# Performance work log

Hardware: AMD Instinct MI355X
Metric: run time of the kernel (lower is better)

Reference implementation:

```python
import jax, jax.numpy as jnp
import numpy as np

K = 3          # opt.k: number of nearest SOM nodes each point is assigned to
SOM_M = 256    # opt.node_num (16x16 SOM grid)


def _point_resnet(x, ws, bs):
    # SO-Net PointResNet: stack of 1x1 conv (relu) layers; the LAST layer takes
    # concat(prev_out, input) as a residual skip connection.
    out = x
    n = len(ws)
    for i in range(n):
        inp = jnp.concatenate([out, x], axis=1) if i == n - 1 else out
        out = jax.nn.relu(jnp.einsum('oc,bcn->bon', ws[i], inp) + bs[i][None, :, None])
    return out


def _encoder(x, sn, node, fp_ws, fp_bs, fn_ws, fn_bs):
    B, _, N = x.shape
    M = node.shape[2]
    xd = jax.lax.stop_gradient(x)      # torch used x.data throughout SOM logic
    nd = jax.lax.stop_gradient(node)
    # squared distances point->node: B,N,M
    x2 = jnp.sum(xd * xd, axis=1)
    n2 = jnp.sum(nd * nd, axis=1)
    cross = jnp.einsum('bcn,bcm->bnm', xd, nd)
    d2 = x2[:, :, None] + n2[:, None, :] - 2.0 * cross
    _, knn_idx = jax.lax.top_k(-d2, K)                 # B,N,K nearest SOM nodes
    min_idx = jnp.transpose(knn_idx, (0, 2, 1)).reshape(B, K * N)  # B,kN (k-major, matches x_stack)
    x_stack = jnp.tile(x, (1, 1, K))                   # B,3,kN
    xs_d = jax.lax.stop_gradient(x_stack)
    # mask_row_sum (counts per node) and masked sum == one-hot mask multiply in the original
    counts = jax.vmap(lambda s: jax.ops.segment_sum(jnp.ones(s.shape, jnp.float32), s, num_segments=SOM_M))(min_idx)  # B,M
    sums = jax.vmap(lambda d, s: jax.ops.segment_sum(d, s, num_segments=SOM_M))(jnp.transpose(xs_d, (0, 2, 1)), min_idx)  # B,M,3
    cluster_mean = jnp.transpose(sums, (0, 2, 1)) / (counts[:, None, :] + 1e-5)  # B,3,M (new som_node)
    # centers: per-point gather of its assigned node (sum(mask*node) over M)
    centers = jnp.take_along_axis(cluster_mean, min_idx[:, None, :], axis=2)     # B,3,kN
    x_dec = jax.lax.stop_gradient(x_stack - centers)   # .detach() in original
    first = _point_resnet(x_dec, fp_ws, fp_bs)         # B,384,kN
    # index_max + gather: per (b,c,node) max over assigned points; empty nodes -> point index 0
    node_max = jax.vmap(lambda d, s: jax.ops.segment_max(d, s, num_segments=SOM_M))(jnp.transpose(first, (0, 2, 1)), min_idx)  # B,M,C
    node_max = jnp.transpose(node_max, (0, 2, 1))      # B,C,M
    has_pts = counts > 0                               # mask_row_max
    fallback = first[:, :, 0:1]                        # gather index 0 for empty nodes
    masked_max = jnp.where(has_pts[:, None, :], node_max, fallback)  # B,384,M
    final_in = jnp.concatenate([cluster_mean, masked_max], axis=1)   # B,387,M
    final = _point_resnet(final_in, fn_ws, fn_bs)      # B,1024,M
    return jnp.max(final, axis=2)                      # B,1024 global feature


def setup_inputs() -> dict:
    key = jax.random.key(0)
    ks = jax.random.split(key, 24)
    B, N, M = 8, 4096, SOM_M
    inp = {
        'x': jax.random.normal(ks[0], (B, 3, N), jnp.float32),
        'sn': jax.random.normal(ks[1], (B, 3, N), jnp.float32),
        'node': jax.random.normal(ks[2], (B, 3, M), jnp.float32),
        'node_knn_I': jax.random.randint(ks[3], (B, M, 1), 0, M),
    }
    fp_dims = [(3, 64), (64, 128), (128, 256), (256 + 3, 384)]
    fn_dims = [(387, 512), (512, 512), (512, 768), (768 + 387, 1024)]
    i = 4
    for j, (cin, cout) in enumerate(fp_dims):
        inp[f'fp_w{j}'] = jax.random.normal(ks[i], (cout, cin), jnp.float32) * np.float32(np.sqrt(2.0 / cin)); i += 1
        inp[f'fp_b{j}'] = jnp.zeros((cout,), jnp.float32)
    for j, (cin, cout) in enumerate(fn_dims):
        inp[f'fn_w{j}'] = jax.random.normal(ks[i], (cout, cin), jnp.float32) * np.float32(np.sqrt(2.0 / cin)); i += 1
        inp[f'fn_b{j}'] = jnp.zeros((cout,), jnp.float32)
    return inp


def reference(x, sn, node, node_knn_I,
              fp_w0, fp_b0, fp_w1, fp_b1, fp_w2, fp_b2, fp_w3, fp_b3,
              fn_w0, fn_b0, fn_w1, fn_b1, fn_w2, fn_b2, fn_w3, fn_b3):
    fp_ws = [fp_w0, fp_w1, fp_w2, fp_w3]
    fp_bs = [fp_b0, fp_b1, fp_b2, fp_b3]
    fn_ws = [fn_w0, fn_w1, fn_w2, fn_w3]
    fn_bs = [fn_b0, fn_b1, fn_b2, fn_b3]
    # node_knn_I only used when som_k >= 2 (KNNModule); som_k=1 here.
    return _encoder(x, sn, node, fp_ws, fp_bs, fn_ws, fn_bs)
```

## Files before the change

### kernel.cpp

```cpp
#include <hip/hip_runtime.h>
#include <math.h>

#define B_   8
#define N_   4096
#define M_   256
#define KNN_ 3

#define OFF_COUNTS   0
#define OFF_CM       8192
#define OFF_NODEMAX  14336
#define OFF_H0       14336
#define OFF_FIRST0   800768
#define OFF_KNN      807944
#define OFF_CAT      807944
#define OFF_SORTED   906248
#define OFF_MSORT    1004552
#define OFF_FIN2     2020360
#define OFF_H1       2020360
#define OFF_WBF      2544648
#define OFF_W3X      3661832
#define O_W0 0
#define O_W1 2048
#define O_W2 10240
#define O_W3 43008
#define O_V0 153600
#define O_V1 366592
#define O_V2 628736
#define O_V3 1021952
#define W_TOTAL 2234368

typedef short  bf16x8 __attribute__((ext_vector_type(8)));
typedef float  f32x4  __attribute__((ext_vector_type(4)));
typedef float  f32x16 __attribute__((ext_vector_type(16)));

__device__ __forceinline__ unsigned short f2b(float f) {
    unsigned u = __float_as_uint(f);
    return (unsigned short)((u + 0x7FFFu + ((u >> 16) & 1u)) >> 16);
}
__device__ __forceinline__ unsigned cvt2(float lo, float hi) {
    unsigned r;
    asm("v_cvt_pk_bf16_f32 %0, %1, %2" : "=v"(r) : "v"(lo), "v"(hi));
    return r;
}
__device__ __forceinline__ f32x16 zero16() {
    f32x16 z;
    #pragma unroll
    for (int i = 0; i < 16; i++) z[i] = 0.f;
    return z;
}

__global__ __launch_bounds__(256) void knn_setup(
        const float* __restrict__ x, const float* __restrict__ node,
        int* __restrict__ knn,
        const float* s0, const float* s1, const float* s2, const float* s3,
        const float* s4, const float* s5, const float* s6, const float* s7,
        unsigned short* __restrict__ dst, float* __restrict__ w3x) {
    __shared__ float nd0[M_], nd1[M_], nd2[M_], nn2[M_];
    int t = threadIdx.x;
    if (blockIdx.x < 128) {
        int b = blockIdx.x >> 4, xblk = blockIdx.x & 15;
        {
            float c0 = node[(b * 3 + 0) * M_ + t];
            float c1 = node[(b * 3 + 1) * M_ + t];
            float c2 = node[(b * 3 + 2) * M_ + t];
            nd0[t] = c0; nd1[t] = c1; nd2[t] = c2;
            nn2[t] = c0 * c0 + c1 * c1 + c2 * c2;
        }
        __syncthreads();
        int n = xblk * 256 + t;
        float x0 = x[(b * 3 + 0) * N_ + n];
        float x1 = x[(b * 3 + 1) * N_ + n];
        float x2 = x[(b * 3 + 2) * N_ + n];
        float xx = x0 * x0 + x1 * x1 + x2 * x2;
        float d0 = 1e30f, d1 = 1e30f, d2b = 1e30f;
        int i0 = 0, i1 = 0, i2 = 0;
        for (int m = 0; m < M_; m++) {
            float cross = x0 * nd0[m] + x1 * nd1[m] + x2 * nd2[m];
            float d = xx + nn2[m] - 2.f * cross;
            bool c0 = d < d0, c1 = d < d1, c2 = d < d2b;
            d2b = c1 ? d1 : (c2 ? d : d2b);
            i2  = c1 ? i1 : (c2 ? m : i2);
            d1  = c0 ? d0 : (c1 ? d : d1);
            i1  = c0 ? i0 : (c1 ? m : i1);
            d0  = c0 ? d  : d0;
            i0  = c0 ? m  : i0;
        }
        int base = (b * N_ + n) * 3;
        knn[base + 0] = i0; knn[base + 1] = i1; knn[base + 2] = i2;
    } else {
        int i = (blockIdx.x - 128) * 256 + t;
        int st = (gridDim.x - 128) * 256;
        for (int j = i; j < 1536; j += st) {
            int ch = j >> 2, c = j & 3;
            w3x[j] = (c < 3) ? s3[ch * 259 + 256 + c] : 0.f;
        }
        for (; i < W_TOTAL; i += st) {
            unsigned short v;
            if (i < O_W1) {
                int loc = i, co = loc >> 5, k = loc & 31;
                v = (k < 3) ? f2b(s0[co * 3 + k]) : (unsigned short)0;
            } else if (i < O_W2) {
                int loc = i - O_W1, co = loc >> 6, k = loc & 63;
                v = f2b(s1[co * 64 + k]);
            } else if (i < O_W3) {
                int loc = i - O_W2, co = loc >> 7, k = loc & 127;
                v = f2b(s2[co * 128 + k]);
            } else if (i < O_V0) {
                int loc = i - O_W3, co = loc / 288u, k = loc - co * 288;
                v = (k < 259) ? f2b(s3[co * 259 + k]) : (unsigned short)0;
            } else if (i < O_V1) {
                int loc = i - O_V0, co = loc / 416u, k = loc - co * 416;
                v = (k < 387) ? f2b(s4[co * 387 + k]) : (unsigned short)0;
            } else if (i < O_V2) {
                int loc = i - O_V1, co = loc >> 9, k = loc & 511;
                v = f2b(s5[co * 512 + k]);
            } else if (i < O_V3) {
                int loc = i - O_V2, co = loc >> 9, k = loc & 511;
                v = f2b(s6[co * 512 + k]);
            } else {
                int loc = i - O_V3, co = loc / 1184u, k = loc - co * 1184;
                v = (k < 1155) ? f2b(s7[co * 1155 + k]) : (unsigned short)0;
            }
            dst[i] = v;
        }
    }
}

__global__ __launch_bounds__(256) void prep(const float* __restrict__ x,
        const int* __restrict__ knn, float* __restrict__ counts_g,
        float* __restrict__ cm, int* __restrict__ sorted, int* __restrict__ msort) {
    __shared__ float hs0[256], hs1[256], hs2[256];
    __shared__ int hc[256], tmp[256], offsL[257], cur[256];
    int t = threadIdx.x, b = blockIdx.x;
    hs0[t] = 0.f; hs1[t] = 0.f; hs2[t] = 0.f; hc[t] = 0; cur[t] = 0;
    __syncthreads();
    for (int e = t; e < KNN_ * N_; e += 256) {
        int n = e & (N_ - 1), k = e >> 12;
        int m = knn[(b * N_ + n) * 3 + k];
        (void)k;
        atomicAdd(&hc[m], 1);
        atomicAdd(&hs0[m], x[(b * 3 + 0) * N_ + n]);
        atomicAdd(&hs1[m], x[(b * 3 + 1) * N_ + n]);
        atomicAdd(&hs2[m], x[(b * 3 + 2) * N_ + n]);
    }
    __syncthreads();
    int v = hc[t];
    float cnt = (float)v;
    counts_g[b * M_ + t] = cnt;
    float inv = 1.f / (cnt + 1e-5f);
    cm[(b * 3 + 0) * M_ + t] = hs0[t] * inv;
    cm[(b * 3 + 1) * M_ + t] = hs1[t] * inv;
    cm[(b * 3 + 2) * M_ + t] = hs2[t] * inv;
    tmp[t] = v;
    __syncthreads();
    for (int off = 1; off < 256; off <<= 1) {
        int u = (t >= off) ? tmp[t - off] : 0;
        __syncthreads();
        tmp[t] += u;
        __syncthreads();
    }
    offsL[t] = tmp[t] - v;
    if (t == 255) offsL[256] = tmp[255];
    __syncthreads();
    for (int e = t; e < KNN_ * N_; e += 256) {
        int n = e & (N_ - 1), k = e >> 12;
        int m = knn[(b * N_ + n) * 3 + k];
        int pos = atomicAdd(&cur[m], 1);
        int dst = offsL[m] + pos;
        sorted[b * (KNN_ * N_) + dst] = e;
        msort[b * (KNN_ * N_) + dst] = m;
    }
}

template<int KS, int INS, int OUTS, int CTW>
__device__ __forceinline__ void layerB(const unsigned short* __restrict__ Wg,
        const float* __restrict__ bias, const unsigned short* actin,
        unsigned short* actout, int wave, int lane) {
    int r = lane & 15, g = lane >> 4;
    bf16x8 bfr[4][KS];
    #pragma unroll
    for (int pt = 0; pt < 4; pt++) {
        const unsigned short* arow = actin + (pt * 16 + r) * INS + g * 8;
        #pragma unroll
        for (int ks = 0; ks < KS; ks++)
            bfr[pt][ks] = *(const bf16x8*)(arow + ks * 32);
    }
    #pragma unroll
    for (int c = 0; c < CTW; c++) {
        int ct = wave * CTW + c;
        const unsigned short* wrow = Wg + (ct * 16 + r) * (KS * 32) + g * 8;
        f32x4 acc[4];
        #pragma unroll
        for (int pt = 0; pt < 4; pt++) acc[pt] = (f32x4){0.f, 0.f, 0.f, 0.f};
        #pragma unroll
        for (int ks = 0; ks < KS; ks++) {
            bf16x8 wv = *(const bf16x8*)(wrow + ks * 32);
            #pragma unroll
            for (int pt = 0; pt < 4; pt++)
                acc[pt] = __builtin_amdgcn_mfma_f32_16x16x32_bf16(wv, bfr[pt][ks], acc[pt], 0, 0, 0);
        }
        f32x4 b4 = *(const f32x4*)(bias + ct * 16 + g * 4);
        #pragma unroll
        for (int pt = 0; pt < 4; pt++) {
            uint2 s;
            s.x = cvt2(fmaxf(acc[pt][0] + b4[0], 0.f), fmaxf(acc[pt][1] + b4[1], 0.f));
            s.y = cvt2(fmaxf(acc[pt][2] + b4[2], 0.f), fmaxf(acc[pt][3] + b4[3], 0.f));
            *(uint2*)(actout + (pt * 16 + r) * OUTS + ct * 16 + g * 4) = s;
        }
    }
}

__global__ __launch_bounds__(256, 3) void mlp1m(
        const float* __restrict__ x, const float* __restrict__ cm,
        const int* __restrict__ sorted, const int* __restrict__ msort,
        const unsigned short* __restrict__ wb, const float4* __restrict__ w3x,
        const float* __restrict__ bb0, const float* __restrict__ bb1,
        const float* __restrict__ bb2, const float* __restrict__ bb3,
        float* __restrict__ node_max, float* __restrict__ first0) {
    __shared__ __align__(16) char smem[50688];
    unsigned short* inb = (unsigned short*)smem;
    unsigned short* a1  = (unsigned short*)smem;
    unsigned short* a0  = (unsigned short*)(smem + 16896);
    unsigned short* cat = (unsigned short*)(smem + 16896);
    __shared__ float4 xdf[64];
    __shared__ int segm[65], segstart[66];
    __shared__ int nseg, p0loc;
    int t = threadIdx.x, b = blockIdx.y, lane = t & 63, wave = t >> 6;
    int e0 = blockIdx.x * 64;
    for (int e = t; e < 1280; e += 256) ((unsigned*)inb)[e] = 0u;
    __syncthreads();
    if (t < 64) {
        int p = t;
        if (p == 0) p0loc = -1;
        int j = sorted[b * 12288 + e0 + p];
        int m = msort[b * 12288 + e0 + p];
        int n = j & (N_ - 1);
        float xd0 = x[(b * 3 + 0) * N_ + n] - cm[(b * 3 + 0) * M_ + m];
        float xd1 = x[(b * 3 + 1) * N_ + n] - cm[(b * 3 + 1) * M_ + m];
        float xd2 = x[(b * 3 + 2) * N_ + n] - cm[(b * 3 + 2) * M_ + m];
        xdf[p] = make_float4(xd0, xd1, xd2, 0.f);
        inb[p * 40 + 0] = f2b(xd0);
        inb[p * 40 + 1] = f2b(xd1);
        inb[p * 40 + 2] = f2b(xd2);
        int prev = __shfl_up(m, 1);
        bool flag = (p == 0) || (m != prev);
        unsigned long long mk = __ballot(flag);
        int sid = __popcll(mk & ((1ull << p) - 1ull));
        if (flag) { segstart[sid] = p; segm[sid] = m; }
        if (p == 63) { int ns2 = __popcll(mk); nseg = ns2; segstart[ns2] = 64; }
        if (j == 0) p0loc = p;
    }
    __syncthreads();
    layerB<1, 40, 72, 1>(wb + O_W0, bb0, inb, a0, wave, lane);
    __syncthreads();
    layerB<2, 72, 132, 2>(wb + O_W1, bb1, a0, a1, wave, lane);
    __syncthreads();
    layerB<4, 132, 264, 4>(wb + O_W2, bb2, a1, cat, wave, lane);
    __syncthreads();
    int l31 = lane & 31, half = lane >> 5;
    f32x16 acc[6];
    #pragma unroll
    for (int q = 0; q < 6; q++) acc[q] = zero16();
    {
        const unsigned short* arow0 = cat + l31 * 264 + half * 8;
        const unsigned short* arow1 = cat + (32 + l31) * 264 + half * 8;
        const unsigned short* wrowb = wb + O_W3 + (wave * 96 + l31) * 288 + half * 8;
        #pragma unroll
        for (int ks = 0; ks < 16; ks++) {
            bf16x8 aA = *(const bf16x8*)(arow0 + ks * 16);
            bf16x8 aB = *(const bf16x8*)(arow1 + ks * 16);
            #pragma unroll
            for (int c3 = 0; c3 < 3; c3++) {
                bf16x8 wv = *(const bf16x8*)(wrowb + c3 * 32 * 288 + ks * 16);
                acc[c3 * 2 + 0] = __builtin_amdgcn_mfma_f32_32x32x16_bf16(aA, wv, acc[c3 * 2 + 0], 0, 0, 0);
                acc[c3 * 2 + 1] = __builtin_amdgcn_mfma_f32_32x32x16_bf16(aB, wv, acc[c3 * 2 + 1], 0, 0, 0);
            }
        }
    }
    int ns = nseg, p0l = p0loc;
    float bias3[3]; float4 wx3[3];
    #pragma unroll
    for (int c3 = 0; c3 < 3; c3++) {
        bias3[c3] = bb3[(wave * 3 + c3) * 32 + l31];
        wx3[c3]   = w3x[(wave * 3 + c3) * 32 + l31];
    }
    #pragma unroll
    for (int ph = 0; ph < 2; ph++) {
        #pragma unroll
        for (int rg = 0; rg < 16; rg++) {
            int row = ph * 32 + (rg & 3) + 8 * (rg >> 2) + 4 * half;
            float4 xv = xdf[row];
            #pragma unroll
            for (int c3 = 0; c3 < 3; c3++) {
                float s = acc[c3 * 2 + ph][rg] + bias3[c3]
                        + wx3[c3].x * xv.x + wx3[c3].y * xv.y + wx3[c3].z * xv.z;
                acc[c3 * 2 + ph][rg] = fmaxf(s, 0.f);
            }
        }
    }
    if (p0l >= 0) {
        #pragma unroll
        for (int ph = 0; ph < 2; ph++)
            #pragma unroll
            for (int rg = 0; rg < 16; rg++) {
                int row = ph * 32 + (rg & 3) + 8 * (rg >> 2) + 4 * half;
                if (row == p0l) {
                    #pragma unroll
                    for (int c3 = 0; c3 < 3; c3++)
                        first0[b * 384 + (wave * 3 + c3) * 32 + l31] = acc[c3 * 2 + ph][rg];
                }
            }
    }
    for (int s = 0; s < ns; s++) {
        int s0 = segstart[s], s1 = segstart[s + 1];
        float m0 = 0.f, m1 = 0.f, m2 = 0.f;
        if (s0 < 32) {
            #pragma unroll
            for (int rg = 0; rg < 16; rg++) {
                int row = (rg & 3) + 8 * (rg >> 2) + 4 * half;
                bool in = (row >= s0) && (row < s1);
                m0 = fmaxf(m0, in ? acc[0][rg] : 0.f);
                m1 = fmaxf(m1, in ? acc[2][rg] : 0.f);
                m2 = fmaxf(m2, in ? acc[4][rg] : 0.f);
            }
        }
        if (s1 > 32) {
            #pragma unroll
            for (int rg = 0; rg < 16; rg++) {
                int row = 32 + (rg & 3) + 8 * (rg >> 2) + 4 * half;
                bool in = (row >= s0) && (row < s1);
                m0 = fmaxf(m0, in ? acc[1][rg] : 0.f);
                m1 = fmaxf(m1, in ? acc[3][rg] : 0.f);
                m2 = fmaxf(m2, in ? acc[5][rg] : 0.f);
            }
        }
        m0 = fmaxf(m0, __shfl_xor(m0, 32));
        m1 = fmaxf(m1, __shfl_xor(m1, 32));
        m2 = fmaxf(m2, __shfl_xor(m2, 32));
        if (lane < 32) {
            float* dstp = &node_max[(size_t)(b * M_ + segm[s]) * 384 + wave * 96];
            atomicMax((int*)(dstp + l31),      __float_as_int(m0));
            atomicMax((int*)(dstp + 32 + l31), __float_as_int(m1));
            atomicMax((int*)(dstp + 64 + l31), __float_as_int(m2));
        }
    }
}

__global__ void build_fin2(const float* __restrict__ cm, const float* __restrict__ counts,
                           const float* __restrict__ nmax, const float* __restrict__ first0,
                           unsigned short* __restrict__ fin2, unsigned short* __restrict__ cat) {
    int tot = 2048 * 416;
    int i = blockIdx.x * blockDim.x + threadIdx.x;
    int st = gridDim.x * blockDim.x;
    for (; i < tot; i += st) {
        int n = i / 416, ch = i - n * 416;
        int b = n >> 8, m = n & 255;
        float v = 0.f;
        if (ch < 3) v = cm[(b * 3 + ch) * M_ + m];
        else if (ch < 387)
            v = (counts[n] > 0.f) ? nmax[(size_t)n * 384 + (ch - 3)]
                                  : first0[b * 384 + (ch - 3)];
        unsigned short u = f2b(v);
        fin2[n * 416 + ch] = u;
        cat[(size_t)n * 1184 + 768 + ch] = u;
    }
}

template<int KS, int CTQ>
__global__ __launch_bounds__(256, 2) void nlayer4(const unsigned short* __restrict__ W,
        const float* __restrict__ bias, const unsigned short* __restrict__ actin,
        unsigned short* __restrict__ actout, int outs) {
    int wave = threadIdx.x >> 6, lane = threadIdx.x & 63;
    int id = blockIdx.x * 4 + wave;
    int nt = id / CTQ, cq = id - nt * CTQ;
    int r = lane & 15, g = lane >> 4;
    const unsigned short* arow = actin + (size_t)(nt * 16 + r) * (KS * 32) + g * 8;
    bf16x8 afr[KS];
    #pragma unroll
    for (int ks = 0; ks < KS; ks++) afr[ks] = *(const bf16x8*)(arow + ks * 32);
    const unsigned short* w0 = W + (cq * 64 + r) * (KS * 32) + g * 8;
    f32x4 acc[4];
    #pragma unroll
    for (int c = 0; c < 4; c++) acc[c] = (f32x4){0.f, 0.f, 0.f, 0.f};
    #pragma unroll
    for (int ks = 0; ks < KS; ks++) {
        #pragma unroll
        for (int c = 0; c < 4; c++) {
            bf16x8 wv = *(const bf16x8*)(w0 + c * 16 * KS * 32 + ks * 32);
            acc[c] = __builtin_amdgcn_mfma_f32_16x16x32_bf16(wv, afr[ks], acc[c], 0, 0, 0);
        }
    }
    #pragma unroll
    for (int c = 0; c < 4; c++) {
        f32x4 b4 = *(const f32x4*)(bias + cq * 64 + c * 16 + g * 4);
        uint2 s;
        s.x = cvt2(fmaxf(acc[c][0] + b4[0], 0.f), fmaxf(acc[c][1] + b4[1], 0.f));
        s.y = cvt2(fmaxf(acc[c][2] + b4[2], 0.f), fmaxf(acc[c][3] + b4[3], 0.f));
        *(uint2*)(actout + (size_t)(nt * 16 + r) * outs + cq * 64 + c * 16 + g * 4) = s;
    }
}

__global__ __launch_bounds__(256) void nlayer_max_s(const unsigned short* __restrict__ W,
        const float* __restrict__ bias, const unsigned short* __restrict__ actin,
        float* __restrict__ out) {
    int wave = threadIdx.x >> 6, lane = threadIdx.x & 63;
    int id = blockIdx.x * 4 + wave;
    int nt = id >> 5, cp = id & 31;
    int r = lane & 15, g = lane >> 4;
    const unsigned short* arow = actin + (size_t)(nt * 16 + r) * 1184 + g * 8;
    const unsigned short* w0 = W + (size_t)(cp * 32 + r) * 1184 + g * 8;
    const unsigned short* w1 = w0 + 16 * 1184;
    f32x4 a0 = {0.f, 0.f, 0.f, 0.f}, a1 = {0.f, 0.f, 0.f, 0.f};
    #pragma unroll 4
    for (int ks = 0; ks < 37; ks++) {
        bf16x8 av = *(const bf16x8*)(arow + ks * 32);
        a0 = __builtin_amdgcn_mfma_f32_16x16x32_bf16(*(const bf16x8*)(w0 + ks * 32), av, a0, 0, 0, 0);
        a1 = __builtin_amdgcn_mfma_f32_16x16x32_bf16(*(const bf16x8*)(w1 + ks * 32), av, a1, 0, 0, 0);
    }
    int b = nt >> 4;
    #pragma unroll
    for (int c = 0; c < 2; c++) {
        f32x4 acc = c ? a1 : a0;
        f32x4 b4 = *(const f32x4*)(bias + cp * 32 + c * 16 + g * 4);
        #pragma unroll
        for (int i = 0; i < 4; i++) {
            float v = fmaxf(acc[i] + b4[i], 0.f);
            v = fmaxf(v, __shfl_xor(v, 1));
            v = fmaxf(v, __shfl_xor(v, 2));
            v = fmaxf(v, __shfl_xor(v, 4));
            v = fmaxf(v, __shfl_xor(v, 8));
            if (r == 0)
                atomicMax((int*)&out[b * 1024 + cp * 32 + c * 16 + g * 4 + i],
                          __float_as_int(v));
        }
    }
}

extern "C" void kernel_launch(void* const* d_in, const int* in_sizes, int n_in,
                              void* d_out, int out_size, void* d_ws, size_t ws_size,
                              hipStream_t stream) {
    (void)in_sizes; (void)n_in; (void)out_size; (void)ws_size;
    const float* x    = (const float*)d_in[0];
    const float* node = (const float*)d_in[2];
    const float* fpw[4] = {(const float*)d_in[4], (const float*)d_in[6],
                           (const float*)d_in[8], (const float*)d_in[10]};
    const float* fpb[4] = {(const float*)d_in[5], (const float*)d_in[7],
                           (const float*)d_in[9], (const float*)d_in[11]};
    const float* fnw[4] = {(const float*)d_in[12], (const float*)d_in[14],
                           (const float*)d_in[16], (const float*)d_in[18]};
    const float* fnb[4] = {(const float*)d_in[13], (const float*)d_in[15],
                           (const float*)d_in[17], (const float*)d_in[19]};
    float* ws  = (float*)d_ws;
    float* out = (float*)d_out;
    unsigned short* wb   = (unsigned short*)(ws + OFF_WBF);
    unsigned short* fin2 = (unsigned short*)(ws + OFF_FIN2);
    unsigned short* h0   = (unsigned short*)(ws + OFF_H0);
    unsigned short* h1   = (unsigned short*)(ws + OFF_H1);
    unsigned short* catb = (unsigned short*)(ws + OFF_CAT);

    hipMemsetAsync(ws + OFF_NODEMAX, 0, (size_t)(B_ * M_ * 384) * 4, stream);
    hipMemsetAsync(out, 0, (size_t)B_ * 1024 * 4, stream);

    knn_setup<<<128 + 2048, 256, 0, stream>>>(
        x, node, (int*)(ws + OFF_KNN),
        fpw[0], fpw[1], fpw[2], fpw[3], fnw[0], fnw[1], fnw[2], fnw[3],
        wb, ws + OFF_W3X);
    prep<<<B_, 256, 0, stream>>>(
        x, (int*)(ws + OFF_KNN), ws + OFF_COUNTS,
        ws + OFF_CM, (int*)(ws + OFF_SORTED), (int*)(ws + OFF_MSORT));
    mlp1m<<<dim3(KNN_ * N_ / 64, B_), 256, 0, stream>>>(
        x, ws + OFF_CM, (int*)(ws + OFF_SORTED), (int*)(ws + OFF_MSORT), wb,
        (const float4*)(ws + OFF_W3X),
        fpb[0], fpb[1], fpb[2], fpb[3], ws + OFF_NODEMAX, ws + OFF_FIRST0);
    build_fin2<<<3328, 256, 0, stream>>>(
        ws + OFF_CM, ws + OFF_COUNTS, ws + OFF_NODEMAX, ws + OFF_FIRST0, fin2, catb);
    nlayer4<13, 8><<<256,  256, 0, stream>>>(wb + O_V0, fnb[0], fin2, h0, 512);
    nlayer4<16, 8><<<256,  256, 0, stream>>>(wb + O_V1, fnb[1], h0, h1, 512);
    nlayer4<16, 12><<<384, 256, 0, stream>>>(wb + O_V2, fnb[2], h1, catb, 1184);
    nlayer_max_s<<<1024, 256, 0, stream>>>(wb + O_V3, fnb[3], catb, out);
}
```

Before: 236.5 us.

## Move cluster histogram into knn kernel via global atomics; split MLP tiles finer

The per-node counts and coordinate sums are now accumulated with global atomics inside the knn kernel, so prep only normalizes and scans instead of re-reading knn and x over 8 blocks. The workspace memset is widened to zero the counts, sums and node-max buffers together. The fn-layer kernels now compute 32 output channels per wave instead of 64, doubling the grid size for more parallelism at the cost of reloading activation fragments more often. Global float atomics add contention and make summation order nondeterministic.

Measured after the change: 201.3 us. 1.17x faster.

```diff
diff --git a/kernel.cpp b/kernel.cpp
--- a/kernel.cpp
+++ b/kernel.cpp
@@ -7,10 +7,12 @@
 #define KNN_ 3
 
 #define OFF_COUNTS   0
+#define OFF_SUMS     2048
 #define OFF_CM       8192
 #define OFF_NODEMAX  14336
 #define OFF_H0       14336
 #define OFF_FIRST0   800768
+#define ZERO_COUNT   803840
 #define OFF_KNN      807944
 #define OFF_CAT      807944
 #define OFF_SORTED   906248
@@ -51,7 +53,7 @@
 
 __global__ __launch_bounds__(256) void knn_setup(
         const float* __restrict__ x, const float* __restrict__ node,
-        int* __restrict__ knn,
+        int* __restrict__ knn, float* __restrict__ counts, float* __restrict__ sums,
         const float* s0, const float* s1, const float* s2, const float* s3,
         const float* s4, const float* s5, const float* s6, const float* s7,
         unsigned short* __restrict__ dst, float* __restrict__ w3x) {
@@ -87,6 +89,15 @@
         }
         int base = (b * N_ + n) * 3;
         knn[base + 0] = i0; knn[base + 1] = i1; knn[base + 2] = i2;
+        int mm[3] = {i0, i1, i2};
+        #pragma unroll
+        for (int k = 0; k < 3; k++) {
+            int m = mm[k];
+            atomicAdd(&counts[b * M_ + m], 1.f);
+            atomicAdd(&sums[(b * M_ + m) * 3 + 0], x0);
+            atomicAdd(&sums[(b * M_ + m) * 3 + 1], x1);
+            atomicAdd(&sums[(b * M_ + m) * 3 + 2], x2);
+        }
     } else {
         int i = (blockIdx.x - 128) * 256 + t;
         int st = (gridDim.x - 128) * 256;
@@ -126,32 +137,18 @@
     }
 }
 
-__global__ __launch_bounds__(256) void prep(const float* __restrict__ x,
-        const int* __restrict__ knn, float* __restrict__ counts_g,
+__global__ __launch_bounds__(256) void prep(const float* __restrict__ counts,
+        const float* __restrict__ sums, const int* __restrict__ knn,
         float* __restrict__ cm, int* __restrict__ sorted, int* __restrict__ msort) {
-    __shared__ float hs0[256], hs1[256], hs2[256];
-    __shared__ int hc[256], tmp[256], offsL[257], cur[256];
+    __shared__ int tmp[256], offsL[257], cur[256];
     int t = threadIdx.x, b = blockIdx.x;
-    hs0[t] = 0.f; hs1[t] = 0.f; hs2[t] = 0.f; hc[t] = 0; cur[t] = 0;
-    __syncthreads();
-    for (int e = t; e < KNN_ * N_; e += 256) {
-        int n = e & (N_ - 1), k = e >> 12;
-        int m = knn[(b * N_ + n) * 3 + k];
-        (void)k;
-        atomicAdd(&hc[m], 1);
-        atomicAdd(&hs0[m], x[(b * 3 + 0) * N_ + n]);
-        atomicAdd(&hs1[m], x[(b * 3 + 1) * N_ + n]);
-        atomicAdd(&hs2[m], x[(b * 3 + 2) * N_ + n]);
-    }
-    __syncthreads();
-    int v = hc[t];
-    float cnt = (float)v;
-    counts_g[b * M_ + t] = cnt;
+    float cnt = counts[b * M_ + t];
     float inv = 1.f / (cnt + 1e-5f);
-    cm[(b * 3 + 0) * M_ + t] = hs0[t] * inv;
-    cm[(b * 3 + 1) * M_ + t] = hs1[t] * inv;
-    cm[(b * 3 + 2) * M_ + t] = hs2[t] * inv;
-    tmp[t] = v;
+    #pragma unroll
+    for (int c = 0; c < 3; c++)
+        cm[(b * 3 + c) * M_ + t] = sums[(b * M_ + t) * 3 + c] * inv;
+    int v = (int)cnt;
+    tmp[t] = v; cur[t] = 0;
     __syncthreads();
     for (int off = 1; off < 256; off <<= 1) {
         int u = (t >= off) ? tmp[t - off] : 0;
@@ -366,38 +363,35 @@
     }
 }
 
-template<int KS, int CTQ>
-__global__ __launch_bounds__(256, 2) void nlayer4(const unsigned short* __restrict__ W,
+template<int KS, int CTP>
+__global__ __launch_bounds__(256) void nlayer2(const unsigned short* __restrict__ W,
         const float* __restrict__ bias, const unsigned short* __restrict__ actin,
         unsigned short* __restrict__ actout, int outs) {
     int wave = threadIdx.x >> 6, lane = threadIdx.x & 63;
     int id = blockIdx.x * 4 + wave;
-    int nt = id / CTQ, cq = id - nt * CTQ;
+    int nt = id / CTP, cp = id - nt * CTP;
     int r = lane & 15, g = lane >> 4;
     const unsigned short* arow = actin + (size_t)(nt * 16 + r) * (KS * 32) + g * 8;
     bf16x8 afr[KS];
     #pragma unroll
     for (int ks = 0; ks < KS; ks++) afr[ks] = *(const bf16x8*)(arow + ks * 32);
-    const unsigned short* w0 = W + (cq * 64 + r) * (KS * 32) + g * 8;
-    f32x4 acc[4];
-    #pragma unroll
-    for (int c = 0; c < 4; c++) acc[c] = (f32x4){0.f, 0.f, 0.f, 0.f};
+    const unsigned short* w0 = W + (cp * 32 + r) * (KS * 32) + g * 8;
+    const unsigned short* w1 = w0 + 16 * KS * 32;
+    f32x4 aA = {0.f,0.f,0.f,0.f}, aB = {0.f,0.f,0.f,0.f};
     #pragma unroll
     for (int ks = 0; ks < KS; ks++) {
-        #pragma unroll
-        for (int c = 0; c < 4; c++) {
-            bf16x8 wv = *(const bf16x8*)(w0 + c * 16 * KS * 32 + ks * 32);
-            acc[c] = __builtin_amdgcn_mfma_f32_16x16x32_bf16(wv, afr[ks], acc[c], 0, 0, 0);
-        }
-    }
-    #pragma unroll
-    for (int c = 0; c < 4; c++) {
-        f32x4 b4 = *(const f32x4*)(bias + cq * 64 + c * 16 + g * 4);
-        uint2 s;
-        s.x = cvt2(fmaxf(acc[c][0] + b4[0], 0.f), fmaxf(acc[c][1] + b4[1], 0.f));
-        s.y = cvt2(fmaxf(acc[c][2] + b4[2], 0.f), fmaxf(acc[c][3] + b4[3], 0.f));
-        *(uint2*)(actout + (size_t)(nt * 16 + r) * outs + cq * 64 + c * 16 + g * 4) = s;
-    }
+        aA = __builtin_amdgcn_mfma_f32_16x16x32_bf16(*(const bf16x8*)(w0 + ks * 32), afr[ks], aA, 0, 0, 0);
+        aB = __builtin_amdgcn_mfma_f32_16x16x32_bf16(*(const bf16x8*)(w1 + ks * 32), afr[ks], aB, 0, 0, 0);
+    }
+    f32x4 b0 = *(const f32x4*)(bias + cp * 32 + g * 4);
+    f32x4 b1 = *(const f32x4*)(bias + cp * 32 + 16 + g * 4);
+    uint2 s0, s1;
+    s0.x = cvt2(fmaxf(aA[0] + b0[0], 0.f), fmaxf(aA[1] + b0[1], 0.f));
+    s0.y = cvt2(fmaxf(aA[2] + b0[2], 0.f), fmaxf(aA[3] + b0[3], 0.f));
+    s1.x = cvt2(fmaxf(aB[0] + b1[0], 0.f), fmaxf(aB[1] + b1[1], 0.f));
+    s1.y = cvt2(fmaxf(aB[2] + b1[2], 0.f), fmaxf(aB[3] + b1[3], 0.f));
+    *(uint2*)(actout + (size_t)(nt * 16 + r) * outs + cp * 32 + g * 4) = s0;
+    *(uint2*)(actout + (size_t)(nt * 16 + r) * outs + cp * 32 + 16 + g * 4) = s1;
 }
 
 __global__ __launch_bounds__(256) void nlayer_max_s(const unsigned short* __restrict__ W,
@@ -458,15 +452,15 @@
     unsigned short* h1   = (unsigned short*)(ws + OFF_H1);
     unsigned short* catb = (unsigned short*)(ws + OFF_CAT);
 
-    hipMemsetAsync(ws + OFF_NODEMAX, 0, (size_t)(B_ * M_ * 384) * 4, stream);
+    hipMemsetAsync(ws, 0, (size_t)ZERO_COUNT * 4, stream);
     hipMemsetAsync(out, 0, (size_t)B_ * 1024 * 4, stream);
 
     knn_setup<<<128 + 2048, 256, 0, stream>>>(
-        x, node, (int*)(ws + OFF_KNN),
+        x, node, (int*)(ws + OFF_KNN), ws + OFF_COUNTS, ws + OFF_SUMS,
         fpw[0], fpw[1], fpw[2], fpw[3], fnw[0], fnw[1], fnw[2], fnw[3],
         wb, ws + OFF_W3X);
     prep<<<B_, 256, 0, stream>>>(
-        x, (int*)(ws + OFF_KNN), ws + OFF_COUNTS,
+        ws + OFF_COUNTS, ws + OFF_SUMS, (int*)(ws + OFF_KNN),
         ws + OFF_CM, (int*)(ws + OFF_SORTED), (int*)(ws + OFF_MSORT));
     mlp1m<<<dim3(KNN_ * N_ / 64, B_), 256, 0, stream>>>(
         x, ws + OFF_CM, (int*)(ws + OFF_SORTED), (int*)(ws + OFF_MSORT), wb,
@@ -474,8 +468,8 @@
         fpb[0], fpb[1], fpb[2], fpb[3], ws + OFF_NODEMAX, ws + OFF_FIRST0);
     build_fin2<<<3328, 256, 0, stream>>>(
         ws + OFF_CM, ws + OFF_COUNTS, ws + OFF_NODEMAX, ws + OFF_FIRST0, fin2, catb);
-    nlayer4<13, 8><<<256,  256, 0, stream>>>(wb + O_V0, fnb[0], fin2, h0, 512);
-    nlayer4<16, 8><<<256,  256, 0, stream>>>(wb + O_V1, fnb[1], h0, h1, 512);
-    nlayer4<16, 12><<<384, 256, 0, stream>>>(wb + O_V2, fnb[2], h1, catb, 1184);
+    nlayer2<13, 16><<<512,  256, 0, stream>>>(wb + O_V0, fnb[0], fin2, h0, 512);
+    nlayer2<16, 16><<<512,  256, 0, stream>>>(wb + O_V1, fnb[1], h0, h1, 512);
+    nlayer2<16, 24><<<768,  256, 0, stream>>>(wb + O_V2, fnb[2], h1, catb, 1184);
     nlayer_max_s<<<1024, 256, 0, stream>>>(wb + O_V3, fnb[3], catb, out);
 }
```
